# Performance work log

Hardware: AMD Instinct MI355X
Metric: run time of the kernel (lower is better)

The kernel has to match this reference:

```python
import jax, jax.numpy as jnp
import numpy as np

B, N, C, H = 8, 4096, 1024, 16
D = C // H
SCALE = D ** -0.5

def setup_inputs() -> dict:
    key = jax.random.key(0)
    ks = jax.random.split(key, 6)
    s = C ** -0.5
    return {
        "fea": jax.random.normal(ks[0], (B, N, C), jnp.float32),
        "embedding": jax.random.normal(ks[1], (B, 1, C), jnp.float32),
        "Wq": jax.random.normal(ks[2], (C, C), jnp.float32) * s,
        "Wk": jax.random.normal(ks[3], (C, C), jnp.float32) * s,
        "Wv": jax.random.normal(ks[4], (C, C), jnp.float32) * s,
        "Wp": jax.random.normal(ks[5], (C, C), jnp.float32) * s,
        "bp": jnp.zeros((C,), jnp.float32),
    }

def reference(fea, embedding, Wq, Wk, Wv, Wp, bp):
    # q: [B,N,H,D]; k,v: [B,H,D] (kv seq len is 1)
    q = (fea @ Wq.T).reshape(B, N, H, D)
    k = (embedding @ Wk.T).reshape(B, H, D)
    v = (embedding @ Wv.T).reshape(B, H, D)
    # attn scores [B,N,H]: single-token key -> per-head dot product
    attn = jax.nn.sigmoid(jnp.einsum("bnhd,bhd->bnh", q, k) * SCALE)
    # broadcast-weight v over sequence: [B,N,H,D] -> [B,N,C]
    feat = (attn[..., None] * v[:, None, :, :]).reshape(B, N, C)
    feat = feat @ Wp.T + bp
    return feat + fea
```

## Files before the change

### kernel.cpp

```cpp
#include <hip/hip_runtime.h>
#include <hip/hip_bf16.h>
#include <stdint.h>

#define B 8
#define N 4096
#define C 1024
#define H 16
#define D 64

static __device__ __forceinline__ float bf_lo(uint32_t u) {
    union { uint32_t i; float f; } c; c.i = u << 16; return c.f;
}
static __device__ __forceinline__ float bf_hi(uint32_t u) {
    union { uint32_t i; float f; } c; c.i = u & 0xffff0000u; return c.f;
}

__global__ __launch_bounds__(256, 2)
void kv_kernel(const float* __restrict__ emb,
               const float* __restrict__ Wk,
               const float* __restrict__ Wv,
               float* __restrict__ kbuf,
               float* __restrict__ vbuf) {
    int wave = (blockIdx.x * blockDim.x + threadIdx.x) >> 6;
    int lane = threadIdx.x & 63;
    int r = wave;
    const float* Wrow = (r < C) ? (Wk + (size_t)r * C) : (Wv + (size_t)(r - C) * C);
    float4 w4[4];
#pragma unroll
    for (int j = 0; j < 4; ++j) w4[j] = *(const float4*)(Wrow + (lane + 64 * j) * 4);
    float acc[B];
#pragma unroll
    for (int b = 0; b < B; ++b) {
        const float* e = emb + (size_t)b * C;
        float a = 0.f;
#pragma unroll
        for (int j = 0; j < 4; ++j) {
            float4 e4 = *(const float4*)(e + (lane + 64 * j) * 4);
            a += w4[j].x * e4.x + w4[j].y * e4.y + w4[j].z * e4.z + w4[j].w * e4.w;
        }
        acc[b] = a;
    }
#pragma unroll
    for (int off = 32; off; off >>= 1)
#pragma unroll
        for (int b = 0; b < B; ++b) acc[b] += __shfl_xor(acc[b], off, 64);
    if (lane == 0) {
        float* dst = (r < C) ? (kbuf + r) : (vbuf + (r - C));
#pragma unroll
        for (int b = 0; b < B; ++b) dst[b * C] = acc[b];
    }
}

__global__ __launch_bounds__(256)
void wu_kernel(const float* __restrict__ Wq,
               const float* __restrict__ Wp,
               const float* __restrict__ kbuf,
               const float* __restrict__ vbuf,
               __hip_bfloat16* __restrict__ wbuf,
               __hip_bfloat16* __restrict__ ubuf) {
    int id = blockIdx.x;
    int t = threadIdx.x;
    if (id < 64) {
        int h = id >> 2;
        int c = ((id & 3) << 8) + t;
        const float* kk = kbuf + h * D;
        float acc[B];
#pragma unroll
        for (int b = 0; b < B; ++b) acc[b] = 0.f;
#pragma unroll 4
        for (int d = 0; d < D; ++d) {
            float wv = Wq[(size_t)(h * D + d) * C + c];
#pragma unroll
            for (int b = 0; b < B; ++b) acc[b] += kk[(size_t)b * C + d] * wv;
        }
#pragma unroll
        for (int b = 0; b < B; ++b)
            wbuf[(size_t)(b * H + h) * C + c] = __float2bfloat16(acc[b]);
    } else {
        int id2 = id - 64;
        int h = id2 >> 2;
        int cp = ((id2 & 3) << 8) + t;
        const float* vv = vbuf + h * D;
        float aq[4][B];
#pragma unroll
        for (int q = 0; q < 4; ++q)
#pragma unroll
            for (int b = 0; b < B; ++b) aq[q][b] = 0.f;
#pragma unroll
        for (int q = 0; q < 4; ++q) {
#pragma unroll
            for (int m = 0; m < 4; ++m) {
                int d0 = q * 16 + m * 4;
                float4 w4 = *(const float4*)(Wp + (size_t)cp * C + h * D + d0);
#pragma unroll
                for (int b = 0; b < B; ++b) {
                    const float* vb = vv + (size_t)b * C + d0;
                    aq[q][b] += w4.x * vb[0] + w4.y * vb[1]
                              + w4.z * vb[2] + w4.w * vb[3];
                }
            }
        }
#pragma unroll
        for (int b = 0; b < B; ++b)
            ubuf[(size_t)(b * H + h) * C + cp] =
                __float2bfloat16((aq[0][b] + aq[1][b]) + (aq[2][b] + aq[3][b]));
    }
}

__global__ __launch_bounds__(512)
void main_kernel(const float* __restrict__ fea,
                 const __hip_bfloat16* __restrict__ wbuf,
                 const __hip_bfloat16* __restrict__ ubuf,
                 const float* __restrict__ bp,
                 float* __restrict__ out) {
    __shared__ float w_f[H * C];
    __shared__ float u_f[H * C];
    const int b = blockIdx.y;
    const int tile = blockIdx.x;
    const int tid = threadIdx.x;

    {
        const uint32_t* wsrc = (const uint32_t*)(wbuf + (size_t)b * H * C);
        const uint32_t* usrc = (const uint32_t*)(ubuf + (size_t)b * H * C);
#pragma unroll
        for (int i = 0; i < H * C / 2 / 512; ++i) {
            int wi = tid + i * 512;
            uint32_t pw = wsrc[wi];
            uint32_t pu = usrc[wi];
            *(float2*)(w_f + 2 * wi) = make_float2(bf_lo(pw), bf_hi(pw));
            *(float2*)(u_f + 2 * wi) = make_float2(bf_lo(pu), bf_hi(pu));
        }
    }
    __syncthreads();

    const int lane = tid & 63;
    const int wv = tid >> 6;
    const int row0 = tile * 128 + wv * 16;

    float4 bp4[4];
#pragma unroll
    for (int j = 0; j < 4; ++j) bp4[j] = *(const float4*)(bp + 4 * lane + 256 * j);

    const float* fbase = fea + ((size_t)b * N + row0) * C + 4 * lane;
    float* obase = out + ((size_t)b * N + row0) * C + 4 * lane;

    float4 fa[2][4];
#pragma unroll
    for (int r = 0; r < 2; ++r)
#pragma unroll
        for (int j = 0; j < 4; ++j)
            fa[r][j] = *(const float4*)(fbase + (size_t)r * C + 256 * j);

#pragma unroll 1
    for (int g = 0; g < 8; ++g) {
        const int gp = (g < 7) ? g + 1 : g;
        float4 fb[2][4];
#pragma unroll
        for (int r = 0; r < 2; ++r)
#pragma unroll
            for (int j = 0; j < 4; ++j)
                fb[r][j] = *(const float4*)(fbase + (size_t)(2 * gp + r) * C + 256 * j);

        float4 acc[2][4];
#pragma unroll
        for (int r = 0; r < 2; ++r)
#pragma unroll
            for (int j = 0; j < 4; ++j) {
                acc[r][j].x = fa[r][j].x + bp4[j].x;
                acc[r][j].y = fa[r][j].y + bp4[j].y;
                acc[r][j].z = fa[r][j].z + bp4[j].z;
                acc[r][j].w = fa[r][j].w + bp4[j].w;
            }

#pragma unroll 1
        for (int h = 0; h < H; ++h) {
            const float* wrow = w_f + h * C + 4 * lane;
            float s[2];
            s[0] = 0.f; s[1] = 0.f;
#pragma unroll
            for (int j = 0; j < 4; ++j) {
                float4 w4 = *(const float4*)(wrow + 256 * j);
#pragma unroll
                for (int r = 0; r < 2; ++r)
                    s[r] += fa[r][j].x * w4.x + fa[r][j].y * w4.y
                          + fa[r][j].z * w4.z + fa[r][j].w * w4.w;
            }
#pragma unroll
            for (int off = 32; off; off >>= 1)
#pragma unroll
                for (int r = 0; r < 2; ++r) s[r] += __shfl_xor(s[r], off, 64);
#pragma unroll
            for (int r = 0; r < 2; ++r)
                s[r] = 1.f / (1.f + __expf(-0.125f * s[r]));

            const float* urow = u_f + h * C + 4 * lane;
#pragma unroll
            for (int j = 0; j < 4; ++j) {
                float4 u4 = *(const float4*)(urow + 256 * j);
#pragma unroll
                for (int r = 0; r < 2; ++r) {
                    acc[r][j].x += s[r] * u4.x; acc[r][j].y += s[r] * u4.y;
                    acc[r][j].z += s[r] * u4.z; acc[r][j].w += s[r] * u4.w;
                }
            }
        }

#pragma unroll
        for (int r = 0; r < 2; ++r)
#pragma unroll
            for (int j = 0; j < 4; ++j)
                *(float4*)(obase + (size_t)(2 * g + r) * C + 256 * j) = acc[r][j];

#pragma unroll
        for (int r = 0; r < 2; ++r)
#pragma unroll
            for (int j = 0; j < 4; ++j) fa[r][j] = fb[r][j];
    }
}

extern "C" void kernel_launch(void* const* d_in, const int* in_sizes, int n_in,
                              void* d_out, int out_size, void* d_ws, size_t ws_size,
                              hipStream_t stream) {
    const float* fea = (const float*)d_in[0];
    const float* emb = (const float*)d_in[1];
    const float* Wq  = (const float*)d_in[2];
    const float* Wk  = (const float*)d_in[3];
    const float* Wv  = (const float*)d_in[4];
    const float* Wp  = (const float*)d_in[5];
    const float* bp  = (const float*)d_in[6];
    float* out = (float*)d_out;

    char* ws = (char*)d_ws;
    float* kbuf = (float*)ws;
    float* vbuf = (float*)(ws + 32 * 1024);
    __hip_bfloat16* wbuf = (__hip_bfloat16*)(ws + 64 * 1024);
    __hip_bfloat16* ubuf = (__hip_bfloat16*)(ws + 320 * 1024);

    hipLaunchKernelGGL(kv_kernel, dim3(2 * C / 4), dim3(256), 0, stream,
                       emb, Wk, Wv, kbuf, vbuf);
    hipLaunchKernelGGL(wu_kernel, dim3(128), dim3(256), 0, stream,
                       Wq, Wp, kbuf, vbuf, wbuf, ubuf);
    hipLaunchKernelGGL(main_kernel, dim3(N / 128, B), dim3(512), 0, stream,
                       fea, wbuf, ubuf, bp, out);
}
```

Baseline: 291.0 us.

## Keep bf16 tables packed in LDS and double block count for occupancy

The main kernel now stores the w/u projection tables in shared memory as packed bf16 (64KB instead of 128KB) and unpacks them on each read. Blocks handle 64 rows instead of 128, the grid doubles, and launch bounds request 4 blocks per CU. The explicit software prefetch of the next fea rows is removed, so latency hiding depends on higher occupancy. The trade-off is extra ALU work to unpack bf16 in the inner loop and twice as many per-block table loads from global memory.

```diff
diff --git a/kernel.cpp b/kernel.cpp
--- a/kernel.cpp
+++ b/kernel.cpp
@@ -107,35 +107,34 @@
     }
 }
 
-__global__ __launch_bounds__(512)
+__global__ __launch_bounds__(512, 4)
 void main_kernel(const float* __restrict__ fea,
                  const __hip_bfloat16* __restrict__ wbuf,
                  const __hip_bfloat16* __restrict__ ubuf,
                  const float* __restrict__ bp,
                  float* __restrict__ out) {
-    __shared__ float w_f[H * C];
-    __shared__ float u_f[H * C];
+    __shared__ uint32_t w_s[H * C / 2];
+    __shared__ uint32_t u_s[H * C / 2];
     const int b = blockIdx.y;
     const int tile = blockIdx.x;
     const int tid = threadIdx.x;
 
     {
-        const uint32_t* wsrc = (const uint32_t*)(wbuf + (size_t)b * H * C);
-        const uint32_t* usrc = (const uint32_t*)(ubuf + (size_t)b * H * C);
-#pragma unroll
-        for (int i = 0; i < H * C / 2 / 512; ++i) {
-            int wi = tid + i * 512;
-            uint32_t pw = wsrc[wi];
-            uint32_t pu = usrc[wi];
-            *(float2*)(w_f + 2 * wi) = make_float2(bf_lo(pw), bf_hi(pw));
-            *(float2*)(u_f + 2 * wi) = make_float2(bf_lo(pu), bf_hi(pu));
+        const uint4* wsrc = (const uint4*)(wbuf + (size_t)b * H * C);
+        const uint4* usrc = (const uint4*)(ubuf + (size_t)b * H * C);
+        uint4* wdst = (uint4*)w_s;
+        uint4* udst = (uint4*)u_s;
+#pragma unroll
+        for (int i = 0; i < H * C / 8 / 512; ++i) {
+            wdst[tid + i * 512] = wsrc[tid + i * 512];
+            udst[tid + i * 512] = usrc[tid + i * 512];
         }
     }
     __syncthreads();
 
     const int lane = tid & 63;
     const int wv = tid >> 6;
-    const int row0 = tile * 128 + wv * 16;
+    const int row0 = tile * 64 + wv * 8;
 
     float4 bp4[4];
 #pragma unroll
@@ -144,46 +143,40 @@
     const float* fbase = fea + ((size_t)b * N + row0) * C + 4 * lane;
     float* obase = out + ((size_t)b * N + row0) * C + 4 * lane;
 
-    float4 fa[2][4];
-#pragma unroll
-    for (int r = 0; r < 2; ++r)
-#pragma unroll
-        for (int j = 0; j < 4; ++j)
-            fa[r][j] = *(const float4*)(fbase + (size_t)r * C + 256 * j);
-
 #pragma unroll 1
-    for (int g = 0; g < 8; ++g) {
-        const int gp = (g < 7) ? g + 1 : g;
-        float4 fb[2][4];
+    for (int g = 0; g < 4; ++g) {
+        float4 f[2][4];
 #pragma unroll
         for (int r = 0; r < 2; ++r)
 #pragma unroll
             for (int j = 0; j < 4; ++j)
-                fb[r][j] = *(const float4*)(fbase + (size_t)(2 * gp + r) * C + 256 * j);
+                f[r][j] = *(const float4*)(fbase + (size_t)(2 * g + r) * C + 256 * j);
 
         float4 acc[2][4];
 #pragma unroll
         for (int r = 0; r < 2; ++r)
 #pragma unroll
             for (int j = 0; j < 4; ++j) {
-                acc[r][j].x = fa[r][j].x + bp4[j].x;
-                acc[r][j].y = fa[r][j].y + bp4[j].y;
-                acc[r][j].z = fa[r][j].z + bp4[j].z;
-                acc[r][j].w = fa[r][j].w + bp4[j].w;
+                acc[r][j].x = f[r][j].x + bp4[j].x;
+                acc[r][j].y = f[r][j].y + bp4[j].y;
+                acc[r][j].z = f[r][j].z + bp4[j].z;
+                acc[r][j].w = f[r][j].w + bp4[j].w;
             }
 
 #pragma unroll 1
         for (int h = 0; h < H; ++h) {
-            const float* wrow = w_f + h * C + 4 * lane;
+            const uint32_t* wrow = w_s + h * (C / 2) + 2 * lane;
             float s[2];
             s[0] = 0.f; s[1] = 0.f;
 #pragma unroll
             for (int j = 0; j < 4; ++j) {
-                float4 w4 = *(const float4*)(wrow + 256 * j);
+                uint2 p = *(const uint2*)(wrow + 128 * j);
+                float lx = bf_lo(p.x), hx = bf_hi(p.x);
+                float ly = bf_lo(p.y), hy = bf_hi(p.y);
 #pragma unroll
                 for (int r = 0; r < 2; ++r)
-                    s[r] += fa[r][j].x * w4.x + fa[r][j].y * w4.y
-                          + fa[r][j].z * w4.z + fa[r][j].w * w4.w;
+                    s[r] += f[r][j].x * lx + f[r][j].y * hx
+                          + f[r][j].z * ly + f[r][j].w * hy;
             }
 #pragma unroll
             for (int off = 32; off; off >>= 1)
@@ -193,14 +186,16 @@
             for (int r = 0; r < 2; ++r)
                 s[r] = 1.f / (1.f + __expf(-0.125f * s[r]));
 
-            const float* urow = u_f + h * C + 4 * lane;
+            const uint32_t* urow = u_s + h * (C / 2) + 2 * lane;
 #pragma unroll
             for (int j = 0; j < 4; ++j) {
-                float4 u4 = *(const float4*)(urow + 256 * j);
+                uint2 p = *(const uint2*)(urow + 128 * j);
+                float lx = bf_lo(p.x), hx = bf_hi(p.x);
+                float ly = bf_lo(p.y), hy = bf_hi(p.y);
 #pragma unroll
                 for (int r = 0; r < 2; ++r) {
-                    acc[r][j].x += s[r] * u4.x; acc[r][j].y += s[r] * u4.y;
-                    acc[r][j].z += s[r] * u4.z; acc[r][j].w += s[r] * u4.w;
+                    acc[r][j].x += s[r] * lx; acc[r][j].y += s[r] * hx;
+                    acc[r][j].z += s[r] * ly; acc[r][j].w += s[r] * hy;
                 }
             }
         }
@@ -210,11 +205,6 @@
 #pragma unroll
             for (int j = 0; j < 4; ++j)
                 *(float4*)(obase + (size_t)(2 * g + r) * C + 256 * j) = acc[r][j];
-
-#pragma unroll
-        for (int r = 0; r < 2; ++r)
-#pragma unroll
-            for (int j = 0; j < 4; ++j) fa[r][j] = fb[r][j];
     }
 }
 
@@ -240,6 +230,6 @@
                        emb, Wk, Wv, kbuf, vbuf);
     hipLaunchKernelGGL(wu_kernel, dim3(128), dim3(256), 0, stream,
                        Wq, Wp, kbuf, vbuf, wbuf, ubuf);
-    hipLaunchKernelGGL(main_kernel, dim3(N / 128, B), dim3(512), 0, stream,
+    hipLaunchKernelGGL(main_kernel, dim3(N / 64, B), dim3(512), 0, stream,
                        fea, wbuf, ubuf, bp, out);
 }
```

Result: no change. 286.1 us (-1.7%).

## Double main kernel block to 1024 threads, drop software prefetch, fold scale into W

Applied to the files above, without the earlier changes.

Each main_kernel block now has 1024 threads, so each wave handles 8 rows instead of 16, and launch bounds ask for more resident waves. The explicit next-row register prefetch is removed, relying on higher occupancy to hide fea load latency. The 0.125 softmax scale is folded into w_f when it is loaded into shared memory, and the dot-product partials are summed as a tree to shorten the dependency chain. Shared memory use per block stays at 128KB, which may cap blocks per CU regardless of the launch bounds.

```diff
diff --git a/kernel.cpp b/kernel.cpp
--- a/kernel.cpp
+++ b/kernel.cpp
@@ -107,7 +107,7 @@
     }
 }
 
-__global__ __launch_bounds__(512)
+__global__ __launch_bounds__(1024, 4)
 void main_kernel(const float* __restrict__ fea,
                  const __hip_bfloat16* __restrict__ wbuf,
                  const __hip_bfloat16* __restrict__ ubuf,
@@ -123,11 +123,12 @@
         const uint32_t* wsrc = (const uint32_t*)(wbuf + (size_t)b * H * C);
         const uint32_t* usrc = (const uint32_t*)(ubuf + (size_t)b * H * C);
 #pragma unroll
-        for (int i = 0; i < H * C / 2 / 512; ++i) {
-            int wi = tid + i * 512;
+        for (int i = 0; i < H * C / 2 / 1024; ++i) {
+            int wi = tid + i * 1024;
             uint32_t pw = wsrc[wi];
             uint32_t pu = usrc[wi];
-            *(float2*)(w_f + 2 * wi) = make_float2(bf_lo(pw), bf_hi(pw));
+            *(float2*)(w_f + 2 * wi) =
+                make_float2(0.125f * bf_lo(pw), 0.125f * bf_hi(pw));
             *(float2*)(u_f + 2 * wi) = make_float2(bf_lo(pu), bf_hi(pu));
         }
     }
@@ -135,7 +136,7 @@
 
     const int lane = tid & 63;
     const int wv = tid >> 6;
-    const int row0 = tile * 128 + wv * 16;
+    const int row0 = tile * 128 + wv * 8;
 
     float4 bp4[4];
 #pragma unroll
@@ -144,54 +145,49 @@
     const float* fbase = fea + ((size_t)b * N + row0) * C + 4 * lane;
     float* obase = out + ((size_t)b * N + row0) * C + 4 * lane;
 
-    float4 fa[2][4];
-#pragma unroll
-    for (int r = 0; r < 2; ++r)
-#pragma unroll
-        for (int j = 0; j < 4; ++j)
-            fa[r][j] = *(const float4*)(fbase + (size_t)r * C + 256 * j);
-
 #pragma unroll 1
-    for (int g = 0; g < 8; ++g) {
-        const int gp = (g < 7) ? g + 1 : g;
-        float4 fb[2][4];
+    for (int g = 0; g < 4; ++g) {
+        float4 f[2][4];
 #pragma unroll
         for (int r = 0; r < 2; ++r)
 #pragma unroll
             for (int j = 0; j < 4; ++j)
-                fb[r][j] = *(const float4*)(fbase + (size_t)(2 * gp + r) * C + 256 * j);
+                f[r][j] = *(const float4*)(fbase + (size_t)(2 * g + r) * C + 256 * j);
 
         float4 acc[2][4];
 #pragma unroll
         for (int r = 0; r < 2; ++r)
 #pragma unroll
             for (int j = 0; j < 4; ++j) {
-                acc[r][j].x = fa[r][j].x + bp4[j].x;
-                acc[r][j].y = fa[r][j].y + bp4[j].y;
-                acc[r][j].z = fa[r][j].z + bp4[j].z;
-                acc[r][j].w = fa[r][j].w + bp4[j].w;
+                acc[r][j].x = f[r][j].x + bp4[j].x;
+                acc[r][j].y = f[r][j].y + bp4[j].y;
+                acc[r][j].z = f[r][j].z + bp4[j].z;
+                acc[r][j].w = f[r][j].w + bp4[j].w;
             }
 
 #pragma unroll 1
         for (int h = 0; h < H; ++h) {
             const float* wrow = w_f + h * C + 4 * lane;
-            float s[2];
-            s[0] = 0.f; s[1] = 0.f;
+            float sp[2][4];
 #pragma unroll
             for (int j = 0; j < 4; ++j) {
                 float4 w4 = *(const float4*)(wrow + 256 * j);
 #pragma unroll
                 for (int r = 0; r < 2; ++r)
-                    s[r] += fa[r][j].x * w4.x + fa[r][j].y * w4.y
-                          + fa[r][j].z * w4.z + fa[r][j].w * w4.w;
-            }
+                    sp[r][j] = f[r][j].x * w4.x + f[r][j].y * w4.y
+                             + f[r][j].z * w4.z + f[r][j].w * w4.w;
+            }
+            float s[2];
+#pragma unroll
+            for (int r = 0; r < 2; ++r)
+                s[r] = (sp[r][0] + sp[r][1]) + (sp[r][2] + sp[r][3]);
 #pragma unroll
             for (int off = 32; off; off >>= 1)
 #pragma unroll
                 for (int r = 0; r < 2; ++r) s[r] += __shfl_xor(s[r], off, 64);
 #pragma unroll
             for (int r = 0; r < 2; ++r)
-                s[r] = 1.f / (1.f + __expf(-0.125f * s[r]));
+                s[r] = 1.f / (1.f + __expf(-s[r]));
 
             const float* urow = u_f + h * C + 4 * lane;
 #pragma unroll
@@ -210,11 +206,6 @@
 #pragma unroll
             for (int j = 0; j < 4; ++j)
                 *(float4*)(obase + (size_t)(2 * g + r) * C + 256 * j) = acc[r][j];
-
-#pragma unroll
-        for (int r = 0; r < 2; ++r)
-#pragma unroll
-            for (int j = 0; j < 4; ++j) fa[r][j] = fb[r][j];
     }
 }
 
@@ -240,6 +231,6 @@
                        emb, Wk, Wv, kbuf, vbuf);
     hipLaunchKernelGGL(wu_kernel, dim3(128), dim3(256), 0, stream,
                        Wq, Wp, kbuf, vbuf, wbuf, ubuf);
-    hipLaunchKernelGGL(main_kernel, dim3(N / 128, B), dim3(512), 0, stream,
+    hipLaunchKernelGGL(main_kernel, dim3(N / 128, B), dim3(1024), 0, stream,
                        fea, wbuf, ubuf, bp, out);
 }
```

Result: no change. 289.1 us (-0.6%).
